# Performance work log

Measured on AMD Instinct MI355X. Metric: run time of the kernel, lower is better.

## Reference

```python
import jax, jax.numpy as jnp
import numpy as np

HEAD_NUM = 16

def setup_inputs() -> dict:
    key = jax.random.key(0)
    kq, kk, kv = jax.random.split(key, 3)
    shape = (4, 2048, 1024)  # [B, N, C]
    return {
        "query_layer": jax.random.normal(kq, shape, dtype=jnp.float32),
        "key_layer": jax.random.normal(kk, shape, dtype=jnp.float32),
        "value_layer": jax.random.normal(kv, shape, dtype=jnp.float32),
    }

def _split_heads(x, h):
    B, N, C = x.shape
    return x.reshape(B, N, h, C // h).transpose(0, 2, 1, 3)  # [B,H,N,d]

def reference(query_layer, key_layer, value_layer):
    B, N, C = query_layer.shape
    h = HEAD_NUM
    d = C // h
    q = _split_heads(query_layer, h)
    k = _split_heads(key_layer, h)
    v = _split_heads(value_layer, h)
    scores = jnp.einsum('bhnd,bhmd->bhnm', q, k) / jnp.sqrt(jnp.asarray(d, q.dtype))
    probs = jax.nn.softmax(scores, axis=-1)
    ctx = jnp.einsum('bhnm,bhmd->bhnd', probs, v)
    return ctx.transpose(0, 2, 1, 3).reshape(B, N, C)
```

## Files before the change

kernel.cpp:

```cpp
#include <hip/hip_runtime.h>
#include <hip/hip_bf16.h>

#define B_   4
#define N_   2048
#define C_   1024
#define NT   32
#define QSCALE 0.18033688011112042f

typedef __attribute__((ext_vector_type(8)))  short short8;
typedef __attribute__((ext_vector_type(4)))  float f32x4;
typedef __attribute__((ext_vector_type(16))) float f32x16;
typedef __attribute__((ext_vector_type(2)))  int   int2v;

__device__ __forceinline__ unsigned short f2bf(float x) {
    union { __hip_bfloat16 h; unsigned short u; } c;
    c.h = __float2bfloat16(x);
    return c.u;
}
__device__ __forceinline__ float fast_exp2(float x) {
    float r; asm("v_exp_f32 %0, %1" : "=v"(r) : "v"(x)); return r;
}
__device__ __forceinline__ int cvtpk(float a, float b) {
    int r; asm("v_cvt_pk_bf16_f32 %0, %1, %2" : "=v"(r) : "v"(a), "v"(b)); return r;
}

__global__ __launch_bounds__(256) void prepack(
    const float* __restrict__ K, const float* __restrict__ V,
    unsigned short* __restrict__ Kt, unsigned short* __restrict__ Vt)
{
    __shared__ __align__(16) unsigned short kl[4096];
    __shared__ __align__(16) unsigned short vl[4096];
    const int L = blockIdx.x;
    const int xcd = L & 7;
    const int j = L >> 3;
    const int head = xcd + 8 * (j >> 5);
    const int t = j & 31;
    const int b = head >> 4, h = head & 15;
    const int tid = threadIdx.x;
    const int r = tid >> 2, cb = tid & 3;
    const size_t head_off = (size_t)b * N_ * C_ + (size_t)h * 64;
    const int kv0 = t * 64;
    const int blk_out = head * NT + t;

    {
        const float* src = K + head_off + (size_t)(kv0 + r) * C_ + cb * 16;
        f32x4 x0 = *(const f32x4*)(src);
        f32x4 x1 = *(const f32x4*)(src + 4);
        f32x4 x2 = *(const f32x4*)(src + 8);
        f32x4 x3 = *(const f32x4*)(src + 12);
        short8 p0, p1;
        #pragma unroll
        for (int i = 0; i < 4; ++i) {
            p0[i] = (short)f2bf(x0[i]); p0[i + 4] = (short)f2bf(x1[i]);
            p1[i] = (short)f2bf(x2[i]); p1[i + 4] = (short)f2bf(x3[i]);
        }
        const int swz = (r & 7) << 3;
        *(short8*)&kl[r * 64 + ((cb * 16) ^ swz)]     = p0;
        *(short8*)&kl[r * 64 + ((cb * 16 + 8) ^ swz)] = p1;
    }
    {
        const float* src = V + head_off + (size_t)(kv0 + r) * C_ + cb * 16;
        f32x4 y0 = *(const f32x4*)(src);
        f32x4 y1 = *(const f32x4*)(src + 4);
        f32x4 y2 = *(const f32x4*)(src + 8);
        f32x4 y3 = *(const f32x4*)(src + 12);
        #pragma unroll
        for (int i = 0; i < 4; ++i) {
            int d0 = cb * 16 + i;
            vl[d0 * 64 + (r ^ ((d0 & 7) << 3))] = f2bf(y0[i]);
            int d1 = cb * 16 + 4 + i;
            vl[d1 * 64 + (r ^ ((d1 & 7) << 3))] = f2bf(y1[i]);
            int d2 = cb * 16 + 8 + i;
            vl[d2 * 64 + (r ^ ((d2 & 7) << 3))] = f2bf(y2[i]);
            int d3 = cb * 16 + 12 + i;
            vl[d3 * 64 + (r ^ ((d3 & 7) << 3))] = f2bf(y3[i]);
        }
    }
    __syncthreads();
    #pragma unroll
    for (int cc = 0; cc < 2; ++cc) {
        const int c  = tid + cc * 256;
        const int f  = c >> 6;
        const int ln = c & 63;
        const int row = (f & 1) * 32 + (ln & 31);
        const int col = (f >> 1) * 16 + (ln >> 5) * 8;
        const int sw  = (row & 7) << 3;
        short8 kk = *(const short8*)&kl[row * 64 + (col ^ sw)];
        short8 vv = *(const short8*)&vl[row * 64 + (col ^ sw)];
        *(short8*)&Kt[(size_t)blk_out * 4096 + c * 8] = kk;
        *(short8*)&Vt[(size_t)blk_out * 4096 + c * 8] = vv;
    }
}

#define MFMA32(A, B, C) __builtin_amdgcn_mfma_f32_32x32x16_bf16((A), (B), (C), 0, 0, 0)

#define TILE_BODY(T, PO0, PO1, PO2, PO3, PI0, PI1, PI2, PI3, FIRST)            \
{                                                                              \
    asm volatile("s_waitcnt vmcnt(0)" ::: "memory");                           \
    __syncthreads();                                                           \
    if ((T) + 1 < NT) stageK((T) + 1, cur ^ 1);                                \
    const unsigned short* kl = &klds[cur][0];                                  \
    f32x16 s0, s1;                                                             \
    {                                                                          \
        const float nm = (FIRST) ? 0.0f : -m_r;   \
        _Pragma("unroll")                                                      \
        for (int r = 0; r < 16; ++r) { s0[r] = nm; s1[r] = nm; }               \
    }                                                                          \
    __builtin_amdgcn_s_setprio(1);                                             \
    {                                                                          \
        short8 kf0 = *(const short8*)&kl[0 * 1024 + lofs];                     \
        short8 kf1 = *(const short8*)&kl[0 * 1024 + 512 + lofs];               \
        s0 = MFMA32(kf0, qfrag[0], s0);                                        \
        s1 = MFMA32(kf1, qfrag[0], s1);                                        \
        kf0 = *(const short8*)&kl[1 * 1024 + lofs];                            \
        kf1 = *(const short8*)&kl[1 * 1024 + 512 + lofs];                      \
        s0 = MFMA32(kf0, qfrag[1], s0);                                        \
        s1 = MFMA32(kf1, qfrag[1], s1);                                        \
        kf0 = *(const short8*)&kl[2 * 1024 + lofs];                            \
        kf1 = *(const short8*)&kl[2 * 1024 + 512 + lofs];                      \
        s0 = MFMA32(kf0, qfrag[2], s0);                                        \
        s1 = MFMA32(kf1, qfrag[2], s1);                                        \
        kf0 = *(const short8*)&kl[3 * 1024 + lofs];                            \
        kf1 = *(const short8*)&kl[3 * 1024 + 512 + lofs];                      \
        s0 = MFMA32(kf0, qfrag[3], s0);                                        \
        s1 = MFMA32(kf1, qfrag[3], s1);                                        \
    }                                                                          \
    if (!(FIRST)) {      \
        o0 = MFMA32(vr0, PI0, o0);  o1 = MFMA32(vr1, PI0, o1);                 \
        o0 = MFMA32(vr2, PI1, o0);  o1 = MFMA32(vr3, PI1, o1);                 \
        o0 = MFMA32(vr4, PI2, o0);  o1 = MFMA32(vr5, PI2, o1);                 \
        o0 = MFMA32(vr6, PI3, o0);  o1 = MFMA32(vr7, PI3, o1);                 \
    }                                                                          \
    __builtin_amdgcn_s_setprio(0);                                             \
    {                \
        const unsigned short* vtp = vbase + (size_t)(T) * 4096 + lofs;         \
        vr0 = *(const short8*)(vtp);                                           \
        vr1 = *(const short8*)(vtp + 512);                                     \
        vr2 = *(const short8*)(vtp + 1024);                                    \
        vr3 = *(const short8*)(vtp + 1536);                                    \
        vr4 = *(const short8*)(vtp + 2048);                                    \
        vr5 = *(const short8*)(vtp + 2560);                                    \
        vr6 = *(const short8*)(vtp + 3072);                                    \
        vr7 = *(const short8*)(vtp + 3584);                                    \
    }                                                                          \
    float mx[8];                                                               \
    _Pragma("unroll")                                                          \
    for (int r = 0; r < 8; ++r)                                                \
        mx[r] = fmaxf(fmaxf(s0[r], s0[r + 8]), fmaxf(s1[r], s1[r + 8]));       \
    _Pragma("unroll")                                                          \
    for (int st = 4; st; st >>= 1) {                                           \
        _Pragma("unroll")                                                      \
        for (int r = 0; r < st; ++r) mx[r] = fmaxf(mx[r], mx[r + st]);         \
    }                                                                          \
    int2v msw = __builtin_amdgcn_permlane32_swap(                              \
        __float_as_int(mx[0]), __float_as_int(mx[0]), false, false);           \
    const float rmp = fmaxf(__int_as_float(msw[0]), __int_as_float(msw[1]));   \
    if (FIRST) {                                                               \
        m_r = rmp;                                                             \
        _Pragma("unroll")                                                      \
        for (int r = 0; r < 16; ++r) { s0[r] -= rmp; s1[r] -= rmp; }           \
    } else if (!__all(rmp <= 8.0f)) {             \
        const float d = fmaxf(rmp, 0.0f);                                      \
        const float corr = fast_exp2(-d);                                      \
        m_r += d;                                                              \
        l_half *= corr;                                                        \
        _Pragma("unroll")                                                      \
        for (int r = 0; r < 16; ++r) {                                         \
            s0[r] -= d; s1[r] -= d;                                            \
            o0[r] *= corr; o1[r] *= corr;                                      \
        }                                                                      \
    }                                                                          \
    _Pragma("unroll")                                                          \
    for (int r = 0; r < 16; ++r) {                                             \
        s0[r] = fast_exp2(s0[r]);                                              \
        s1[r] = fast_exp2(s1[r]);                                              \
    }                                                                          \
    {                              \
        int w0, w1, w2, w3; int2v sA, sB;                                      \
        union { int i[4]; short8 v; } u;                                       \
        w0 = cvtpk(s0[0], s0[1]);  w1 = cvtpk(s0[2], s0[3]);                   \
        w2 = cvtpk(s0[4], s0[5]);  w3 = cvtpk(s0[6], s0[7]);                   \
        sA = __builtin_amdgcn_permlane32_swap(w0, w2, false, false);           \
        sB = __builtin_amdgcn_permlane32_swap(w1, w3, false, false);           \
        u.i[0] = sA[0]; u.i[1] = sB[0]; u.i[2] = sA[1]; u.i[3] = sB[1];        \
        PO0 = u.v;                                                             \
        w0 = cvtpk(s0[8], s0[9]);  w1 = cvtpk(s0[10], s0[11]);                 \
        w2 = cvtpk(s0[12], s0[13]); w3 = cvtpk(s0[14], s0[15]);                \
        sA = __builtin_amdgcn_permlane32_swap(w0, w2, false, false);           \
        sB = __builtin_amdgcn_permlane32_swap(w1, w3, false, false);           \
        u.i[0] = sA[0]; u.i[1] = sB[0]; u.i[2] = sA[1]; u.i[3] = sB[1];        \
        PO1 = u.v;                                                             \
        w0 = cvtpk(s1[0], s1[1]);  w1 = cvtpk(s1[2], s1[3]);                   \
        w2 = cvtpk(s1[4], s1[5]);  w3 = cvtpk(s1[6], s1[7]);                   \
        sA = __builtin_amdgcn_permlane32_swap(w0, w2, false, false);           \
        sB = __builtin_amdgcn_permlane32_swap(w1, w3, false, false);           \
        u.i[0] = sA[0]; u.i[1] = sB[0]; u.i[2] = sA[1]; u.i[3] = sB[1];        \
        PO2 = u.v;                                                             \
        w0 = cvtpk(s1[8], s1[9]);  w1 = cvtpk(s1[10], s1[11]);                 \
        w2 = cvtpk(s1[12], s1[13]); w3 = cvtpk(s1[14], s1[15]);                \
        sA = __builtin_amdgcn_permlane32_swap(w0, w2, false, false);           \
        sB = __builtin_amdgcn_permlane32_swap(w1, w3, false, false);           \
        u.i[0] = sA[0]; u.i[1] = sB[0]; u.i[2] = sA[1]; u.i[3] = sB[1];        \
        PO3 = u.v;                                                             \
    }                                                                          \
    float aa[8];                                                               \
    _Pragma("unroll")                                                          \
    for (int r = 0; r < 8; ++r) aa[r] = (s0[r] + s0[r + 8]) + (s1[r] + s1[r + 8]); \
    _Pragma("unroll")                                                          \
    for (int st = 4; st; st >>= 1) {                                           \
        _Pragma("unroll")                                                      \
        for (int r = 0; r < st; ++r) aa[r] += aa[r + st];                      \
    }                                                                          \
    l_half += aa[0];                                                           \
    cur ^= 1;                                                                  \
}

__global__ __launch_bounds__(256, 3) void attn_fwd(
    const float* __restrict__ Q, const unsigned short* __restrict__ Kt,
    const unsigned short* __restrict__ Vt, float* __restrict__ O)
{
    __shared__ __align__(16) unsigned short klds[2][4096];

    const int L = blockIdx.x;
    const int xcd = L & 7;
    const int j = L >> 3;
    const int head = xcd + 8 * (j >> 4);
    const int qt = j & 15;
    const int b = head >> 4, h = head & 15;

    const int tid  = threadIdx.x;
    const int wave = tid >> 6;
    const int lane = tid & 63;
    const int l31  = lane & 31;
    const int hi   = lane >> 5;

    const unsigned short* kbase = Kt + (size_t)head * (NT * 4096);
    const unsigned short* vbase = Vt + (size_t)head * (NT * 4096);
    const float* qp = Q + (size_t)b * N_ * C_ + (size_t)h * 64;
    float*       op = O + (size_t)b * N_ * C_ + (size_t)h * 64;

    const int qrow = qt * 128 + wave * 32 + l31;
    short8 qfrag[4];
    {
        const float* qr = qp + (size_t)qrow * C_ + hi * 8;
        #pragma unroll
        for (int ks = 0; ks < 4; ++ks) {
            f32x4 x0 = *(const f32x4*)(qr + ks * 16);
            f32x4 x1 = *(const f32x4*)(qr + ks * 16 + 4);
            short8 a;
            #pragma unroll
            for (int i = 0; i < 4; ++i) {
                a[i]     = (short)f2bf(x0[i] * QSCALE);
                a[i + 4] = (short)f2bf(x1[i] * QSCALE);
            }
            qfrag[ks] = a;
        }
    }

    f32x16 o0 = {}, o1 = {};
    float m_r = 0.0f, l_half = 0.0f;

    const int lofs = lane * 8;

    auto stageK = [&](int t, int buf) {
        const unsigned short* kg = kbase + (size_t)t * 4096 + wave * 1024 + lofs;
        __builtin_amdgcn_global_load_lds((const __attribute__((address_space(1))) void*)kg,
            (__attribute__((address_space(3))) void*)&klds[buf][wave * 1024], 16, 0, 0);
        __builtin_amdgcn_global_load_lds((const __attribute__((address_space(1))) void*)(kg + 512),
            (__attribute__((address_space(3))) void*)&klds[buf][wave * 1024 + 512], 16, 0, 0);
    };

    int cur = 0;
    short8 pA0, pA1, pA2, pA3, pB0, pB1, pB2, pB3;
    short8 vr0, vr1, vr2, vr3, vr4, vr5, vr6, vr7;

    stageK(0, 0);

    TILE_BODY(0, pA0, pA1, pA2, pA3, pB0, pB1, pB2, pB3, true)
    for (int t = 1; t < NT - 1; t += 2) {
        TILE_BODY(t,     pB0, pB1, pB2, pB3, pA0, pA1, pA2, pA3, false)
        TILE_BODY(t + 1, pA0, pA1, pA2, pA3, pB0, pB1, pB2, pB3, false)
    }
    TILE_BODY(NT - 1, pB0, pB1, pB2, pB3, pA0, pA1, pA2, pA3, false)

    __builtin_amdgcn_s_setprio(1);
    o0 = MFMA32(vr0, pB0, o0);  o1 = MFMA32(vr1, pB0, o1);
    o0 = MFMA32(vr2, pB1, o0);  o1 = MFMA32(vr3, pB1, o1);
    o0 = MFMA32(vr4, pB2, o0);  o1 = MFMA32(vr5, pB2, o1);
    o0 = MFMA32(vr6, pB3, o0);  o1 = MFMA32(vr7, pB3, o1);
    __builtin_amdgcn_s_setprio(0);

    int2v lsw = __builtin_amdgcn_permlane32_swap(
        __float_as_int(l_half), __float_as_int(l_half), false, false);
    const float l_r = __int_as_float(lsw[0]) + __int_as_float(lsw[1]);
    const float inv = 1.0f / l_r;

    float* orow = op + (size_t)qrow * C_;
    #pragma unroll
    for (int bb = 0; bb < 4; ++bb) {
        f32x4 w0, w1;
        #pragma unroll
        for (int i = 0; i < 4; ++i) {
            w0[i] = o0[4 * bb + i] * inv;
            w1[i] = o1[4 * bb + i] * inv;
        }
        *(f32x4*)(orow + 8 * bb + 4 * hi)      = w0;
        *(f32x4*)(orow + 32 + 8 * bb + 4 * hi) = w1;
    }
}

extern "C" void kernel_launch(void* const* d_in, const int* in_sizes, int n_in,
                              void* d_out, int out_size, void* d_ws, size_t ws_size,
                              hipStream_t stream) {
    const float* q = (const float*)d_in[0];
    const float* k = (const float*)d_in[1];
    const float* v = (const float*)d_in[2];
    float* o = (float*)d_out;
    unsigned short* Kt = (unsigned short*)d_ws;
    unsigned short* Vt = Kt + (size_t)64 * NT * 4096;
    prepack<<<dim3(64 * NT), dim3(256), 0, stream>>>(k, v, Kt, Vt);
    attn_fwd<<<dim3(1024), dim3(256), 0, stream>>>(q, Kt, Vt, o);
}
```

Before: 110.0 us.

## Load K tiles directly into registers and compute row sums via MFMA

Replaces the double-buffered LDS staging of K, along with its per-tile vmcnt wait and block barrier, with per-wave prefetch of the next K tile into registers. Each wave now fetches the whole K tile from global/L2 instead of sharing one LDS copy. The softmax denominator moves from a VALU reduction tree to four extra MFMAs per tile against a ones operand, and the alternating P register sets are collapsed into one. The change trades barrier and LDS overhead for more global load traffic, extra MFMA work and higher VGPR pressure under the 3-blocks-per-CU launch bound.

```diff
diff --git a/kernel.cpp b/kernel.cpp
--- a/kernel.cpp
+++ b/kernel.cpp
@@ -94,12 +94,8 @@
 
 #define MFMA32(A, B, C) __builtin_amdgcn_mfma_f32_32x32x16_bf16((A), (B), (C), 0, 0, 0)
 
-#define TILE_BODY(T, PO0, PO1, PO2, PO3, PI0, PI1, PI2, PI3, FIRST)            \
+#define TILE_BODY(T, FIRST)                                                    \
 {                                                                              \
-    asm volatile("s_waitcnt vmcnt(0)" ::: "memory");                           \
-    __syncthreads();                                                           \
-    if ((T) + 1 < NT) stageK((T) + 1, cur ^ 1);                                \
-    const unsigned short* kl = &klds[cur][0];                                  \
     f32x16 s0, s1;                                                             \
     {                                                                          \
         const float nm = (FIRST) ? 0.0f : -m_r;   \
@@ -107,41 +103,34 @@
         for (int r = 0; r < 16; ++r) { s0[r] = nm; s1[r] = nm; }               \
     }                                                                          \
     __builtin_amdgcn_s_setprio(1);                                             \
-    {                                                                          \
-        short8 kf0 = *(const short8*)&kl[0 * 1024 + lofs];                     \
-        short8 kf1 = *(const short8*)&kl[0 * 1024 + 512 + lofs];               \
-        s0 = MFMA32(kf0, qfrag[0], s0);                                        \
-        s1 = MFMA32(kf1, qfrag[0], s1);                                        \
-        kf0 = *(const short8*)&kl[1 * 1024 + lofs];                            \
-        kf1 = *(const short8*)&kl[1 * 1024 + 512 + lofs];                      \
-        s0 = MFMA32(kf0, qfrag[1], s0);                                        \
-        s1 = MFMA32(kf1, qfrag[1], s1);                                        \
-        kf0 = *(const short8*)&kl[2 * 1024 + lofs];                            \
-        kf1 = *(const short8*)&kl[2 * 1024 + 512 + lofs];                      \
-        s0 = MFMA32(kf0, qfrag[2], s0);                                        \
-        s1 = MFMA32(kf1, qfrag[2], s1);                                        \
-        kf0 = *(const short8*)&kl[3 * 1024 + lofs];                            \
-        kf1 = *(const short8*)&kl[3 * 1024 + 512 + lofs];                      \
-        s0 = MFMA32(kf0, qfrag[3], s0);                                        \
-        s1 = MFMA32(kf1, qfrag[3], s1);                                        \
-    }                                                                          \
-    if (!(FIRST)) {      \
-        o0 = MFMA32(vr0, PI0, o0);  o1 = MFMA32(vr1, PI0, o1);                 \
-        o0 = MFMA32(vr2, PI1, o0);  o1 = MFMA32(vr3, PI1, o1);                 \
-        o0 = MFMA32(vr4, PI2, o0);  o1 = MFMA32(vr5, PI2, o1);                 \
-        o0 = MFMA32(vr6, PI3, o0);  o1 = MFMA32(vr7, PI3, o1);                 \
+    s0 = MFMA32(kr0, qfrag[0], s0);  s1 = MFMA32(kr1, qfrag[0], s1);           \
+    s0 = MFMA32(kr2, qfrag[1], s0);  s1 = MFMA32(kr3, qfrag[1], s1);           \
+    s0 = MFMA32(kr4, qfrag[2], s0);  s1 = MFMA32(kr5, qfrag[2], s1);           \
+    s0 = MFMA32(kr6, qfrag[3], s0);  s1 = MFMA32(kr7, qfrag[3], s1);           \
+    if (!(FIRST)) {     \
+        o0 = MFMA32(vr0, pf0, o0);  o1 = MFMA32(vr1, pf0, o1);                 \
+        o0 = MFMA32(vr2, pf1, o0);  o1 = MFMA32(vr3, pf1, o1);                 \
+        o0 = MFMA32(vr4, pf2, o0);  o1 = MFMA32(vr5, pf2, o1);                 \
+        o0 = MFMA32(vr6, pf3, o0);  o1 = MFMA32(vr7, pf3, o1);                 \
+        lacc = MFMA32(ones_f, pf0, lacc);                                      \
+        lacc = MFMA32(ones_f, pf1, lacc);                                      \
+        lacc = MFMA32(ones_f, pf2, lacc);                                      \
+        lacc = MFMA32(ones_f, pf3, lacc);                                      \
     }                                                                          \
     __builtin_amdgcn_s_setprio(0);                                             \
-    {                \
+    if ((T) + 1 < NT) {     \
+        const unsigned short* kg = kbase + (size_t)((T) + 1) * 4096 + lofs;    \
+        kr0 = *(const short8*)(kg);         kr1 = *(const short8*)(kg + 512);  \
+        kr2 = *(const short8*)(kg + 1024);  kr3 = *(const short8*)(kg + 1536); \
+        kr4 = *(const short8*)(kg + 2048);  kr5 = *(const short8*)(kg + 2560); \
+        kr6 = *(const short8*)(kg + 3072);  kr7 = *(const short8*)(kg + 3584); \
+    }                                                                          \
+    {                           \
         const unsigned short* vtp = vbase + (size_t)(T) * 4096 + lofs;         \
-        vr0 = *(const short8*)(vtp);                                           \
-        vr1 = *(const short8*)(vtp + 512);                                     \
-        vr2 = *(const short8*)(vtp + 1024);                                    \
-        vr3 = *(const short8*)(vtp + 1536);                                    \
-        vr4 = *(const short8*)(vtp + 2048);                                    \
-        vr5 = *(const short8*)(vtp + 2560);                                    \
-        vr6 = *(const short8*)(vtp + 3072);                                    \
-        vr7 = *(const short8*)(vtp + 3584);                                    \
+        vr0 = *(const short8*)(vtp);         vr1 = *(const short8*)(vtp + 512);\
+        vr2 = *(const short8*)(vtp + 1024);  vr3 = *(const short8*)(vtp + 1536);\
+        vr4 = *(const short8*)(vtp + 2048);  vr5 = *(const short8*)(vtp + 2560);\
+        vr6 = *(const short8*)(vtp + 3072);  vr7 = *(const short8*)(vtp + 3584);\
     }                                                                          \
     float mx[8];                                                               \
     _Pragma("unroll")                                                          \
@@ -163,7 +152,7 @@
         const float d = fmaxf(rmp, 0.0f);                                      \
         const float corr = fast_exp2(-d);                                      \
         m_r += d;                                                              \
-        l_half *= corr;                                                        \
+        lacc[0] *= corr;                  \
         _Pragma("unroll")                                                      \
         for (int r = 0; r < 16; ++r) {                                         \
             s0[r] -= d; s1[r] -= d;                                            \
@@ -175,52 +164,40 @@
         s0[r] = fast_exp2(s0[r]);                                              \
         s1[r] = fast_exp2(s1[r]);                                              \
     }                                                                          \
-    {                              \
+    {      \
         int w0, w1, w2, w3; int2v sA, sB;                                      \
         union { int i[4]; short8 v; } u;                                       \
-        w0 = cvtpk(s0[0], s0[1]);  w1 = cvtpk(s0[2], s0[3]);                   \
-        w2 = cvtpk(s0[4], s0[5]);  w3 = cvtpk(s0[6], s0[7]);                   \
+        w0 = cvtpk(s0[0], s0[1]);   w1 = cvtpk(s0[2], s0[3]);                  \
+        w2 = cvtpk(s0[4], s0[5]);   w3 = cvtpk(s0[6], s0[7]);                  \
         sA = __builtin_amdgcn_permlane32_swap(w0, w2, false, false);           \
         sB = __builtin_amdgcn_permlane32_swap(w1, w3, false, false);           \
         u.i[0] = sA[0]; u.i[1] = sB[0]; u.i[2] = sA[1]; u.i[3] = sB[1];        \
-        PO0 = u.v;                                                             \
-        w0 = cvtpk(s0[8], s0[9]);  w1 = cvtpk(s0[10], s0[11]);                 \
+        pf0 = u.v;                                                             \
+        w0 = cvtpk(s0[8], s0[9]);   w1 = cvtpk(s0[10], s0[11]);                \
         w2 = cvtpk(s0[12], s0[13]); w3 = cvtpk(s0[14], s0[15]);                \
         sA = __builtin_amdgcn_permlane32_swap(w0, w2, false, false);           \
         sB = __builtin_amdgcn_permlane32_swap(w1, w3, false, false);           \
         u.i[0] = sA[0]; u.i[1] = sB[0]; u.i[2] = sA[1]; u.i[3] = sB[1];        \
-        PO1 = u.v;                                                             \
-        w0 = cvtpk(s1[0], s1[1]);  w1 = cvtpk(s1[2], s1[3]);                   \
-        w2 = cvtpk(s1[4], s1[5]);  w3 = cvtpk(s1[6], s1[7]);                   \
+        pf1 = u.v;                                                             \
+        w0 = cvtpk(s1[0], s1[1]);   w1 = cvtpk(s1[2], s1[3]);                  \
+        w2 = cvtpk(s1[4], s1[5]);   w3 = cvtpk(s1[6], s1[7]);                  \
         sA = __builtin_amdgcn_permlane32_swap(w0, w2, false, false);           \
         sB = __builtin_amdgcn_permlane32_swap(w1, w3, false, false);           \
         u.i[0] = sA[0]; u.i[1] = sB[0]; u.i[2] = sA[1]; u.i[3] = sB[1];        \
-        PO2 = u.v;                                                             \
-        w0 = cvtpk(s1[8], s1[9]);  w1 = cvtpk(s1[10], s1[11]);                 \
+        pf2 = u.v;                                                             \
+        w0 = cvtpk(s1[8], s1[9]);   w1 = cvtpk(s1[10], s1[11]);                \
         w2 = cvtpk(s1[12], s1[13]); w3 = cvtpk(s1[14], s1[15]);                \
         sA = __builtin_amdgcn_permlane32_swap(w0, w2, false, false);           \
         sB = __builtin_amdgcn_permlane32_swap(w1, w3, false, false);           \
         u.i[0] = sA[0]; u.i[1] = sB[0]; u.i[2] = sA[1]; u.i[3] = sB[1];        \
-        PO3 = u.v;                                                             \
-    }                                                                          \
-    float aa[8];                                                               \
-    _Pragma("unroll")                                                          \
-    for (int r = 0; r < 8; ++r) aa[r] = (s0[r] + s0[r + 8]) + (s1[r] + s1[r + 8]); \
-    _Pragma("unroll")                                                          \
-    for (int st = 4; st; st >>= 1) {                                           \
-        _Pragma("unroll")                                                      \
-        for (int r = 0; r < st; ++r) aa[r] += aa[r + st];                      \
-    }                                                                          \
-    l_half += aa[0];                                                           \
-    cur ^= 1;                                                                  \
+        pf3 = u.v;                                                             \
+    }                                                                          \
 }
 
 __global__ __launch_bounds__(256, 3) void attn_fwd(
     const float* __restrict__ Q, const unsigned short* __restrict__ Kt,
     const unsigned short* __restrict__ Vt, float* __restrict__ O)
 {
-    __shared__ __align__(16) unsigned short klds[2][4096];
-
     const int L = blockIdx.x;
     const int xcd = L & 7;
     const int j = L >> 3;
@@ -257,43 +234,44 @@
         }
     }
 
-    f32x16 o0 = {}, o1 = {};
-    float m_r = 0.0f, l_half = 0.0f;
+    short8 ones_f;
+    #pragma unroll
+    for (int i = 0; i < 8; ++i) ones_f[i] = (short)0x3F80;
+
+    f32x16 o0 = {}, o1 = {}, lacc = {};
+    float m_r = 0.0f;
 
     const int lofs = lane * 8;
 
-    auto stageK = [&](int t, int buf) {
-        const unsigned short* kg = kbase + (size_t)t * 4096 + wave * 1024 + lofs;
-        __builtin_amdgcn_global_load_lds((const __attribute__((address_space(1))) void*)kg,
-            (__attribute__((address_space(3))) void*)&klds[buf][wave * 1024], 16, 0, 0);
-        __builtin_amdgcn_global_load_lds((const __attribute__((address_space(1))) void*)(kg + 512),
-            (__attribute__((address_space(3))) void*)&klds[buf][wave * 1024 + 512], 16, 0, 0);
-    };
-
-    int cur = 0;
-    short8 pA0, pA1, pA2, pA3, pB0, pB1, pB2, pB3;
+    short8 kr0, kr1, kr2, kr3, kr4, kr5, kr6, kr7;
     short8 vr0, vr1, vr2, vr3, vr4, vr5, vr6, vr7;
-
-    stageK(0, 0);
-
-    TILE_BODY(0, pA0, pA1, pA2, pA3, pB0, pB1, pB2, pB3, true)
-    for (int t = 1; t < NT - 1; t += 2) {
-        TILE_BODY(t,     pB0, pB1, pB2, pB3, pA0, pA1, pA2, pA3, false)
-        TILE_BODY(t + 1, pA0, pA1, pA2, pA3, pB0, pB1, pB2, pB3, false)
-    }
-    TILE_BODY(NT - 1, pB0, pB1, pB2, pB3, pA0, pA1, pA2, pA3, false)
+    short8 pf0, pf1, pf2, pf3;
+
+    {
+        const unsigned short* kg = kbase + lofs;
+        kr0 = *(const short8*)(kg);         kr1 = *(const short8*)(kg + 512);
+        kr2 = *(const short8*)(kg + 1024);  kr3 = *(const short8*)(kg + 1536);
+        kr4 = *(const short8*)(kg + 2048);  kr5 = *(const short8*)(kg + 2560);
+        kr6 = *(const short8*)(kg + 3072);  kr7 = *(const short8*)(kg + 3584);
+    }
+
+    TILE_BODY(0, true)
+    for (int t = 1; t < NT; ++t) {
+        TILE_BODY(t, false)
+    }
 
     __builtin_amdgcn_s_setprio(1);
-    o0 = MFMA32(vr0, pB0, o0);  o1 = MFMA32(vr1, pB0, o1);
-    o0 = MFMA32(vr2, pB1, o0);  o1 = MFMA32(vr3, pB1, o1);
-    o0 = MFMA32(vr4, pB2, o0);  o1 = MFMA32(vr5, pB2, o1);
-    o0 = MFMA32(vr6, pB3, o0);  o1 = MFMA32(vr7, pB3, o1);
+    o0 = MFMA32(vr0, pf0, o0);  o1 = MFMA32(vr1, pf0, o1);
+    o0 = MFMA32(vr2, pf1, o0);  o1 = MFMA32(vr3, pf1, o1);
+    o0 = MFMA32(vr4, pf2, o0);  o1 = MFMA32(vr5, pf2, o1);
+    o0 = MFMA32(vr6, pf3, o0);  o1 = MFMA32(vr7, pf3, o1);
+    lacc = MFMA32(ones_f, pf0, lacc);
+    lacc = MFMA32(ones_f, pf1, lacc);
+    lacc = MFMA32(ones_f, pf2, lacc);
+    lacc = MFMA32(ones_f, pf3, lacc);
     __builtin_amdgcn_s_setprio(0);
 
-    int2v lsw = __builtin_amdgcn_permlane32_swap(
-        __float_as_int(l_half), __float_as_int(l_half), false, false);
-    const float l_r = __int_as_float(lsw[0]) + __int_as_float(lsw[1]);
-    const float inv = 1.0f / l_r;
+    const float inv = 1.0f / lacc[0];
 
     float* orow = op + (size_t)qrow * C_;
     #pragma unroll
```

After: 148.5 us. 35.0% more time.

## Compute softmax row sums via MFMA, relax barrier waitcnt, flatten max reduction

Applied to the files above, without the earlier changes.

The row-sum accumulation of probabilities moves from a VALU add-tree plus cross-lane swap to an extra MFMA per P-fragment against an all-ones bf16 operand, accumulating into a new f32x16 register tile. The per-tile full vmcnt(0) wait before the barrier is relaxed to vmcnt(8), so the eight V register loads may still be in flight, with sched_barriers around it, and the initial K stage is synced once before the loop. The max reduction is restructured into a shallower tree. This trades VALU work and waits for extra MFMA issue and 16 more accumulator registers, and the row sum now uses bf16-rounded probabilities, which may affect occupancy and accuracy.

```diff
diff --git a/kernel.cpp b/kernel.cpp
--- a/kernel.cpp
+++ b/kernel.cpp
@@ -96,9 +96,14 @@
 
 #define TILE_BODY(T, PO0, PO1, PO2, PO3, PI0, PI1, PI2, PI3, FIRST)            \
 {                                                                              \
-    asm volatile("s_waitcnt vmcnt(0)" ::: "memory");                           \
-    __syncthreads();                                                           \
+    if ((T) > 0) {         \
+        asm volatile("s_waitcnt vmcnt(8)" ::: "memory");                       \
+        __builtin_amdgcn_sched_barrier(0);                                     \
+        __builtin_amdgcn_s_barrier();                                          \
+        __builtin_amdgcn_sched_barrier(0);                                     \
+    }                                                                          \
     if ((T) + 1 < NT) stageK((T) + 1, cur ^ 1);                                \
+    __builtin_amdgcn_sched_barrier(0);   \
     const unsigned short* kl = &klds[cur][0];                                  \
     f32x16 s0, s1;                                                             \
     {                                                                          \
@@ -125,11 +130,15 @@
         s0 = MFMA32(kf0, qfrag[3], s0);                                        \
         s1 = MFMA32(kf1, qfrag[3], s1);                                        \
     }                                                                          \
-    if (!(FIRST)) {      \
+    if (!(FIRST)) {           \
         o0 = MFMA32(vr0, PI0, o0);  o1 = MFMA32(vr1, PI0, o1);                 \
+        lacc = MFMA32(ones_f, PI0, lacc);                                      \
         o0 = MFMA32(vr2, PI1, o0);  o1 = MFMA32(vr3, PI1, o1);                 \
+        lacc = MFMA32(ones_f, PI1, lacc);                                      \
         o0 = MFMA32(vr4, PI2, o0);  o1 = MFMA32(vr5, PI2, o1);                 \
+        lacc = MFMA32(ones_f, PI2, lacc);                                      \
         o0 = MFMA32(vr6, PI3, o0);  o1 = MFMA32(vr7, PI3, o1);                 \
+        lacc = MFMA32(ones_f, PI3, lacc);                                      \
     }                                                                          \
     __builtin_amdgcn_s_setprio(0);                                             \
     {                \
@@ -145,15 +154,14 @@
     }                                                                          \
     float mx[8];                                                               \
     _Pragma("unroll")                                                          \
-    for (int r = 0; r < 8; ++r)                                                \
-        mx[r] = fmaxf(fmaxf(s0[r], s0[r + 8]), fmaxf(s1[r], s1[r + 8]));       \
-    _Pragma("unroll")                                                          \
-    for (int st = 4; st; st >>= 1) {                                           \
-        _Pragma("unroll")                                                      \
-        for (int r = 0; r < st; ++r) mx[r] = fmaxf(mx[r], mx[r + st]);         \
-    }                                                                          \
+    for (int r = 0; r < 8; ++r)                 \
+        mx[r] = fmaxf(fmaxf(fmaxf(s0[r], s0[r + 8]), s1[r]), s1[r + 8]);       \
+    const float tA = fmaxf(fmaxf(mx[0], mx[1]), mx[2]);                        \
+    const float tB = fmaxf(fmaxf(mx[3], mx[4]), mx[5]);                        \
+    const float tC = fmaxf(mx[6], mx[7]);                                      \
+    const float vmx = fmaxf(fmaxf(tA, tB), tC);                                \
     int2v msw = __builtin_amdgcn_permlane32_swap(                              \
-        __float_as_int(mx[0]), __float_as_int(mx[0]), false, false);           \
+        __float_as_int(vmx), __float_as_int(vmx), false, false);               \
     const float rmp = fmaxf(__int_as_float(msw[0]), __int_as_float(msw[1]));   \
     if (FIRST) {                                                               \
         m_r = rmp;                                                             \
@@ -163,7 +171,7 @@
         const float d = fmaxf(rmp, 0.0f);                                      \
         const float corr = fast_exp2(-d);                                      \
         m_r += d;                                                              \
-        l_half *= corr;                                                        \
+        lacc[0] *= corr;                        \
         _Pragma("unroll")                                                      \
         for (int r = 0; r < 16; ++r) {                                         \
             s0[r] -= d; s1[r] -= d;                                            \
@@ -203,15 +211,6 @@
         u.i[0] = sA[0]; u.i[1] = sB[0]; u.i[2] = sA[1]; u.i[3] = sB[1];        \
         PO3 = u.v;                                                             \
     }                                                                          \
-    float aa[8];                                                               \
-    _Pragma("unroll")                                                          \
-    for (int r = 0; r < 8; ++r) aa[r] = (s0[r] + s0[r + 8]) + (s1[r] + s1[r + 8]); \
-    _Pragma("unroll")                                                          \
-    for (int st = 4; st; st >>= 1) {                                           \
-        _Pragma("unroll")                                                      \
-        for (int r = 0; r < st; ++r) aa[r] += aa[r + st];                      \
-    }                                                                          \
-    l_half += aa[0];                                                           \
     cur ^= 1;                                                                  \
 }
 
@@ -257,8 +256,12 @@
         }
     }
 
-    f32x16 o0 = {}, o1 = {};
-    float m_r = 0.0f, l_half = 0.0f;
+    short8 ones_f;
+    #pragma unroll
+    for (int i = 0; i < 8; ++i) ones_f[i] = (short)0x3F80;
+
+    f32x16 o0 = {}, o1 = {}, lacc = {};
+    float m_r = 0.0f;
 
     const int lofs = lane * 8;
 
@@ -275,6 +278,8 @@
     short8 vr0, vr1, vr2, vr3, vr4, vr5, vr6, vr7;
 
     stageK(0, 0);
+    asm volatile("s_waitcnt vmcnt(0)" ::: "memory");
+    __syncthreads();
 
     TILE_BODY(0, pA0, pA1, pA2, pA3, pB0, pB1, pB2, pB3, true)
     for (int t = 1; t < NT - 1; t += 2) {
@@ -285,15 +290,16 @@
 
     __builtin_amdgcn_s_setprio(1);
     o0 = MFMA32(vr0, pB0, o0);  o1 = MFMA32(vr1, pB0, o1);
+    lacc = MFMA32(ones_f, pB0, lacc);
     o0 = MFMA32(vr2, pB1, o0);  o1 = MFMA32(vr3, pB1, o1);
+    lacc = MFMA32(ones_f, pB1, lacc);
     o0 = MFMA32(vr4, pB2, o0);  o1 = MFMA32(vr5, pB2, o1);
+    lacc = MFMA32(ones_f, pB2, lacc);
     o0 = MFMA32(vr6, pB3, o0);  o1 = MFMA32(vr7, pB3, o1);
+    lacc = MFMA32(ones_f, pB3, lacc);
     __builtin_amdgcn_s_setprio(0);
 
-    int2v lsw = __builtin_amdgcn_permlane32_swap(
-        __float_as_int(l_half), __float_as_int(l_half), false, false);
-    const float l_r = __int_as_float(lsw[0]) + __int_as_float(lsw[1]);
-    const float inv = 1.0f / l_r;
+    const float inv = 1.0f / lacc[0];
 
     float* orow = op + (size_t)qrow * C_;
     #pragma unroll
```

After: 119.8 us. 1.09x slower.

## Give each wave a private K tile in LDS and drop block barriers

Applied to the files above, without the earlier changes.

Each wave now stages the whole K tile into its own LDS slice with eight direct global-to-LDS loads. This replaces the shared double buffer that needed a vmcnt(0) wait plus __syncthreads every tile. Waves can therefore run out of lockstep, and the next tile's K load is issued after the QK MFMAs, with vmcnt(8) counting only the older K loads. In exchange, K traffic from L2 goes up fourfold and LDS per block doubles. Prefetch distance also shrinks to a single buffer per wave, so more K latency may be exposed.

```diff
diff --git a/kernel.cpp b/kernel.cpp
--- a/kernel.cpp
+++ b/kernel.cpp
@@ -96,10 +96,9 @@
 
 #define TILE_BODY(T, PO0, PO1, PO2, PO3, PI0, PI1, PI2, PI3, FIRST)            \
 {                                                                              \
-    asm volatile("s_waitcnt vmcnt(0)" ::: "memory");                           \
-    __syncthreads();                                                           \
-    if ((T) + 1 < NT) stageK((T) + 1, cur ^ 1);                                \
-    const unsigned short* kl = &klds[cur][0];                                  \
+    if ((T) > 0) {    \
+        asm volatile("s_waitcnt vmcnt(8)" ::: "memory");                       \
+    }                                                                          \
     f32x16 s0, s1;                                                             \
     {                                                                          \
         const float nm = (FIRST) ? 0.0f : -m_r;   \
@@ -108,20 +107,20 @@
     }                                                                          \
     __builtin_amdgcn_s_setprio(1);                                             \
     {                                                                          \
-        short8 kf0 = *(const short8*)&kl[0 * 1024 + lofs];                     \
-        short8 kf1 = *(const short8*)&kl[0 * 1024 + 512 + lofs];               \
+        short8 kf0 = *(const short8*)&kl[0 * 512 + lofs8];                     \
+        short8 kf1 = *(const short8*)&kl[1 * 512 + lofs8];                     \
         s0 = MFMA32(kf0, qfrag[0], s0);                                        \
         s1 = MFMA32(kf1, qfrag[0], s1);                                        \
-        kf0 = *(const short8*)&kl[1 * 1024 + lofs];                            \
-        kf1 = *(const short8*)&kl[1 * 1024 + 512 + lofs];                      \
+        kf0 = *(const short8*)&kl[2 * 512 + lofs8];                            \
+        kf1 = *(const short8*)&kl[3 * 512 + lofs8];                            \
         s0 = MFMA32(kf0, qfrag[1], s0);                                        \
         s1 = MFMA32(kf1, qfrag[1], s1);                                        \
-        kf0 = *(const short8*)&kl[2 * 1024 + lofs];                            \
-        kf1 = *(const short8*)&kl[2 * 1024 + 512 + lofs];                      \
+        kf0 = *(const short8*)&kl[4 * 512 + lofs8];                            \
+        kf1 = *(const short8*)&kl[5 * 512 + lofs8];                            \
         s0 = MFMA32(kf0, qfrag[2], s0);                                        \
         s1 = MFMA32(kf1, qfrag[2], s1);                                        \
-        kf0 = *(const short8*)&kl[3 * 1024 + lofs];                            \
-        kf1 = *(const short8*)&kl[3 * 1024 + 512 + lofs];                      \
+        kf0 = *(const short8*)&kl[6 * 512 + lofs8];                            \
+        kf1 = *(const short8*)&kl[7 * 512 + lofs8];                            \
         s0 = MFMA32(kf0, qfrag[3], s0);                                        \
         s1 = MFMA32(kf1, qfrag[3], s1);                                        \
     }                                                                          \
@@ -132,8 +131,9 @@
         o0 = MFMA32(vr6, PI3, o0);  o1 = MFMA32(vr7, PI3, o1);                 \
     }                                                                          \
     __builtin_amdgcn_s_setprio(0);                                             \
+    if ((T) + 1 < NT) stageK((T) + 1);     \
     {                \
-        const unsigned short* vtp = vbase + (size_t)(T) * 4096 + lofs;         \
+        const unsigned short* vtp = vbase + (size_t)(T) * 4096 + lofs8;        \
         vr0 = *(const short8*)(vtp);                                           \
         vr1 = *(const short8*)(vtp + 512);                                     \
         vr2 = *(const short8*)(vtp + 1024);                                    \
@@ -212,14 +212,13 @@
         for (int r = 0; r < st; ++r) aa[r] += aa[r + st];                      \
     }                                                                          \
     l_half += aa[0];                                                           \
-    cur ^= 1;                                                                  \
 }
 
 __global__ __launch_bounds__(256, 3) void attn_fwd(
     const float* __restrict__ Q, const unsigned short* __restrict__ Kt,
     const unsigned short* __restrict__ Vt, float* __restrict__ O)
 {
-    __shared__ __align__(16) unsigned short klds[2][4096];
+    __shared__ __align__(16) unsigned short klds[4][4096];
 
     const int L = blockIdx.x;
     const int xcd = L & 7;
@@ -238,6 +237,21 @@
     const unsigned short* vbase = Vt + (size_t)head * (NT * 4096);
     const float* qp = Q + (size_t)b * N_ * C_ + (size_t)h * 64;
     float*       op = O + (size_t)b * N_ * C_ + (size_t)h * 64;
+
+    const int lofs8 = lane * 8;
+    unsigned short* kl = &klds[wave][0];
+
+    auto stageK = [&](int t) {
+        const unsigned short* kg = kbase + (size_t)t * 4096 + lofs8;
+        #pragma unroll
+        for (int f = 0; f < 8; ++f) {
+            __builtin_amdgcn_global_load_lds(
+                (const __attribute__((address_space(1))) void*)(kg + f * 512),
+                (__attribute__((address_space(3))) void*)&kl[f * 512], 16, 0, 0);
+        }
+    };
+
+    stageK(0);
 
     const int qrow = qt * 128 + wave * 32 + l31;
     short8 qfrag[4];
@@ -260,21 +274,10 @@
     f32x16 o0 = {}, o1 = {};
     float m_r = 0.0f, l_half = 0.0f;
 
-    const int lofs = lane * 8;
-
-    auto stageK = [&](int t, int buf) {
-        const unsigned short* kg = kbase + (size_t)t * 4096 + wave * 1024 + lofs;
-        __builtin_amdgcn_global_load_lds((const __attribute__((address_space(1))) void*)kg,
-            (__attribute__((address_space(3))) void*)&klds[buf][wave * 1024], 16, 0, 0);
-        __builtin_amdgcn_global_load_lds((const __attribute__((address_space(1))) void*)(kg + 512),
-            (__attribute__((address_space(3))) void*)&klds[buf][wave * 1024 + 512], 16, 0, 0);
-    };
-
-    int cur = 0;
     short8 pA0, pA1, pA2, pA3, pB0, pB1, pB2, pB3;
     short8 vr0, vr1, vr2, vr3, vr4, vr5, vr6, vr7;
 
-    stageK(0, 0);
+    asm volatile("s_waitcnt vmcnt(0)" ::: "memory");
 
     TILE_BODY(0, pA0, pA1, pA2, pA3, pB0, pB1, pB2, pB3, true)
     for (int t = 1; t < NT - 1; t += 2) {
```

Measured after the change: 116.8 us. 6.2% more time.
